# Kernel optimization log

Measured on AMD Instinct MI355X. Metric: run time of the kernel, lower is better.

The kernel has to match this reference:

```python
import jax, jax.numpy as jnp
import numpy as np

# dims: batch, samples, agents, obs_dim, action_dim, hidden
B, S, N, D, A, H = 512, 64, 8, 64, 16, 256
IN_DIM = (D + A) * N  # 640


def mish(x):
    return x * jnp.tanh(jax.nn.softplus(x))


def setup_inputs() -> dict:
    key = jax.random.key(0)
    ks = jax.random.split(key, 9)
    u = lambda k, shape, fan_in: jax.random.uniform(
        k, shape, jnp.float32, -1.0 / np.sqrt(fan_in), 1.0 / np.sqrt(fan_in))
    return {
        "state": jax.random.normal(ks[0], (B, N, D), jnp.float32),
        "action": jax.random.normal(ks[1], (B, N, A), jnp.float32),
        "W1": u(ks[2], (IN_DIM, H), IN_DIM),
        "b1": u(ks[3], (H,), IN_DIM),
        "W2": u(ks[4], (H, H), H),
        "b2": u(ks[5], (H,), H),
        "W3": u(ks[6], (H, 1), H),
        "b3": u(ks[7], (1,), H),
        # random grand-coalition permutations of the N agents, per (batch, sample)
        "perm": jnp.argsort(jax.random.uniform(ks[8], (B, S, N)), axis=-1).astype(jnp.int32),
    }


def reference(state, action, W1, b1, W2, b2, W3, b3, perm):
    # subcoalition mask [B,S,N,N]: torch builds one-hot(perm) @ tril(ones),
    # i.e. mask[b,s,i,j] = 1 iff j <= perm[b,s,i]
    subcoal = (jnp.arange(N) <= perm[..., None]).astype(state.dtype)
    # gathered actions in coalition order [B,S,N,A]: act_g[b,s,j] = action[b, perm[b,s,j]]
    act_g = action[jnp.arange(B)[:, None, None], perm]
    # masked subcoalition actions [B,S,N,N,A] -> [B,S,N,N*A]
    act = (act_g[:, :, None, :, :] * subcoal[..., None]).reshape(B, S, N, N * A)
    # flattened global obs broadcast over (sample, agent) axes [B,S,N,N*D]
    obs = jnp.broadcast_to(state.reshape(B, 1, 1, N * D), (B, S, N, N * D))
    x = jnp.concatenate([obs, act], axis=-1)  # [B,S,N,IN_DIM]
    # per-agent loop in torch uses shared q1 weights -> single batched MLP
    h = mish(x @ W1 + b1)
    h = mish(h @ W2 + b2)
    q = h @ W3 + b3                   # [B,S,N,1]
    q1 = q.mean(axis=1).squeeze(-1)   # mean over samples -> [B,N]
    return (q1, q1)
```

## Files before the change

### kernel.cpp

```cpp
#include <hip/hip_runtime.h>

typedef unsigned short ushort_t;
typedef _Float16 half_t;
typedef __attribute__((ext_vector_type(2))) _Float16 half2_t;
typedef __attribute__((ext_vector_type(8))) _Float16 half8_t;
typedef __attribute__((ext_vector_type(2))) __fp16 fp16x2;
typedef __attribute__((ext_vector_type(2))) float fx2;
typedef __attribute__((ext_vector_type(4))) float floatx4;

#define LOG2E 1.4426950408889634f
#define LN2   0.6931471805599453f

__device__ __forceinline__ float exp2_(float x) {
#if __has_builtin(__builtin_amdgcn_exp2f)
    return __builtin_amdgcn_exp2f(x);
#else
    return exp2f(x);
#endif
}

__device__ __forceinline__ half2_t cvt_pk_f16(float a, float b) {
    auto r = __builtin_amdgcn_cvt_pkrtz(a, b);
    return __builtin_bit_cast(half2_t, r);
}

__device__ __forceinline__ float fdot2_(half2_t a, half2_t b) {
#if __has_builtin(__builtin_amdgcn_fdot2)
    return __builtin_amdgcn_fdot2(__builtin_bit_cast(fp16x2, a),
                                  __builtin_bit_cast(fp16x2, b), 0.0f, false);
#else
    return (float)a.x * (float)b.x + (float)a.y * (float)b.y;
#endif
}

__device__ __forceinline__ fx2 mish2(fx2 t0) {
    fx2 one = {1.0f, 1.0f};
    fx2 m2  = {-2.0f, -2.0f};
    fx2 u   = {exp2_(t0.x), exp2_(t0.y)};
    fx2 s   = u + one;
    fx2 wv  = __builtin_elementwise_fma(s, s, one);
    fx2 rr  = {__builtin_amdgcn_rcpf(wv.x), __builtin_amdgcn_rcpf(wv.y)};
    fx2 v   = __builtin_elementwise_fma(rr, m2, one);
    return t0 * v;
}

__device__ __forceinline__ float dpp_sum16(float v) {
    int x = __float_as_int(v);
    v += __int_as_float(__builtin_amdgcn_update_dpp(0, x, 0xB1, 0xF, 0xF, true));
    x = __float_as_int(v);
    v += __int_as_float(__builtin_amdgcn_update_dpp(0, x, 0x4E, 0xF, 0xF, true));
    x = __float_as_int(v);
    v += __int_as_float(__builtin_amdgcn_update_dpp(0, x, 0x124, 0xF, 0xF, true));
    x = __float_as_int(v);
    v += __int_as_float(__builtin_amdgcn_update_dpp(0, x, 0x128, 0xF, 0xF, true));
    return v;
}

__global__ __launch_bounds__(256) void prep_kernel(
        const float* __restrict__ state,
        const float* __restrict__ action,
        const float* __restrict__ W1,
        const float* __restrict__ W2,
        float* __restrict__ obsWp,
        half_t* __restrict__ actW,
        half_t* __restrict__ W2T,
        float* __restrict__ out) {
    int bid = blockIdx.x;
    int t = threadIdx.x;
    if (bid < 512) {
        int bg = bid >> 3;
        int kc = bid & 7;
        int bs = bg * 8;
        const float* w1p = W1 + (size_t)(kc * 64) * 256 + t;
        const float* stp = state + (size_t)bs * 512 + kc * 64;
        float acc[8];
#pragma unroll
        for (int bb = 0; bb < 8; ++bb) acc[bb] = 0.f;
#pragma unroll 4
        for (int f = 0; f < 64; ++f) {
            float w = w1p[f * 256];
#pragma unroll
            for (int bb = 0; bb < 8; ++bb)
                acc[bb] = fmaf(stp[bb * 512 + f], w, acc[bb]);
        }
#pragma unroll
        for (int bb = 0; bb < 8; ++bb)
            obsWp[(size_t)kc * 131072 + (bs + bb) * 256 + t] = acc[bb];
    } else if (bid < 1536) {
        int idx = bid - 512;
        int j = idx & 7;
        int b0 = (idx >> 3) * 4;
        const float* W1a = W1 + (size_t)(512 + j * 16) * 256;
        float wv[16];
#pragma unroll
        for (int a = 0; a < 16; ++a) wv[a] = W1a[a * 256 + t];
#pragma unroll
        for (int bb = 0; bb < 4; ++bb) {
            int b = b0 + bb;
            const float* acp = action + (size_t)b * 128;
            float acc[8];
#pragma unroll
            for (int n = 0; n < 8; ++n) acc[n] = 0.f;
#pragma unroll
            for (int a = 0; a < 16; ++a) {
#pragma unroll
                for (int n = 0; n < 8; ++n)
                    acc[n] = fmaf(acp[n * 16 + a], wv[a], acc[n]);
            }
#pragma unroll
            for (int n = 0; n < 8; ++n)
                actW[(((size_t)b * 8 + n) * 8 + j) * 256 + t] = (half_t)(acc[n] * LOG2E);
        }
    } else {
        int blk = bid - 1536;
        if (blk < 16) {
            out[blk * 512 + t] = 0.0f;
            out[blk * 512 + 256 + t] = 0.0f;
        }
        int n = blk * 8 + (t >> 5);
        int klo = t & 31;
#pragma unroll
        for (int kk = 0; kk < 8; ++kk) {
            int k = kk * 32 + klo;
            W2T[n * 256 + k] = (half_t)W2[k * 256 + n];
        }
    }
}

#define CHUNK_US 528

__global__ __launch_bounds__(512, 4) void main_kernel(
        const float* __restrict__ obsWp, const half_t* __restrict__ actW,
        const half_t* __restrict__ W2T, const int* __restrict__ perm,
        const float* __restrict__ b1, const float* __restrict__ b2,
        const float* __restrict__ W3, const float* __restrict__ b3,
        float* __restrict__ out) {
    __shared__ __align__(16) ushort_t h1[2][32 * CHUNK_US];
    __shared__ __align__(16) float obsb[256];
    __shared__ int perm_s[128];
    __shared__ float qpart[2][8][64];

    int t = threadIdx.x;
    int bid = blockIdx.x;
    int b = (bid & 7) * 64 + ((bid >> 3) & 63);
    int sgp = bid >> 9;
    int s0 = sgp * 16;

    int w = t >> 6;
    int L = t & 63;
    int lo = L & 15;
    int q = L >> 4;

    if (t < 256) {
        float s = b1[t];
#pragma unroll
        for (int c = 0; c < 8; ++c) s += obsWp[(size_t)c * 131072 + b * 256 + t];
        obsb[t] = s * LOG2E;
    } else if (t < 384) {
        perm_s[t - 256] = perm[((size_t)b * 64 + s0) * 8 + (t - 256)];
    }

    const half_t* w2base = W2T + ((size_t)(w * 32 + lo)) * 256 + q * 8;
    half8_t bpre[4];
    bpre[0] = *reinterpret_cast<const half8_t*>(w2base + 0 * 4096 + 0 * 32);
    bpre[1] = *reinterpret_cast<const half8_t*>(w2base + 1 * 4096 + 0 * 32);
    bpre[2] = *reinterpret_cast<const half8_t*>(w2base + 0 * 4096 + 1 * 32);
    bpre[3] = *reinterpret_cast<const half8_t*>(w2base + 1 * 4096 + 1 * 32);

    int g = L >> 1;
    int ksg = g >> 2;
    int qq = g & 3;
    int halfsel = L & 1;
    const half_t* actb = actW + (size_t)b * 64 * 256;
    int dstoff = qq * 128 + halfsel * 4 + ksg * CHUNK_US
               + (w >> 1) * (8 * CHUNK_US) + (w & 1) * 64;

    __syncthreads();

    float4 ob = *reinterpret_cast<const float4*>(obsb + L * 4);

    {
        uint2 av[8];
#pragma unroll
        for (int j = 0; j < 8; ++j) {
            int p = perm_s[(0 * 8 + w) * 8 + j];
            unsigned po = __builtin_amdgcn_readfirstlane((unsigned)((p * 8 + j) * 256));
            av[j] = *reinterpret_cast<const uint2*>(actb + po + L * 4);
        }
        fx2 r01 = {ob.x, ob.y};
        fx2 r23 = {ob.z, ob.w};
        ushort_t* dst0 = h1[0] + dstoff;
#pragma unroll
        for (int j = 0; j < 8; ++j) {
            half2_t a0 = __builtin_bit_cast(half2_t, av[j].x);
            half2_t a1 = __builtin_bit_cast(half2_t, av[j].y);
            r01 += (fx2){(float)a0.x, (float)a0.y};
            r23 += (fx2){(float)a1.x, (float)a1.y};
            fx2 h01 = mish2(r01);
            fx2 h23 = mish2(r23);
            uint2 pk = make_uint2(__builtin_bit_cast(unsigned, cvt_pk_f16(h01.x, h01.y)),
                                  __builtin_bit_cast(unsigned, cvt_pk_f16(h23.x, h23.y)));
            *reinterpret_cast<uint2*>(dst0 + j * 8) = pk;
        }
    }
    __syncthreads();

    floatx4 acc0[4][2];
#pragma unroll
    for (int mt = 0; mt < 4; ++mt)
#pragma unroll
        for (int nt = 0; nt < 2; ++nt) acc0[mt][nt] = (floatx4){0.f, 0.f, 0.f, 0.f};
    {
        uint2 av[8];
#pragma unroll
        for (int j = 0; j < 8; ++j) {
            int p = perm_s[(1 * 8 + w) * 8 + j];
            unsigned po = __builtin_amdgcn_readfirstlane((unsigned)((p * 8 + j) * 256));
            av[j] = *reinterpret_cast<const uint2*>(actb + po + L * 4);
        }
        fx2 r01 = {ob.x, ob.y};
        fx2 r23 = {ob.z, ob.w};
        ushort_t* dst1 = h1[1] + dstoff;
        const ushort_t* h1b0 = h1[0] + L * 8;
#pragma unroll
        for (int ks = 0; ks < 8; ++ks) {
            half8_t afr[4];
#pragma unroll
            for (int mt = 0; mt < 4; ++mt)
                afr[mt] = *reinterpret_cast<const half8_t*>(h1b0 + (mt * 8 + ks) * CHUNK_US);
            half8_t bfr0 = (ks == 0) ? bpre[0] : (ks == 1) ? bpre[2]
                         : *reinterpret_cast<const half8_t*>(w2base + 0 * 4096 + ks * 32);
            half8_t bfr1 = (ks == 0) ? bpre[1] : (ks == 1) ? bpre[3]
                         : *reinterpret_cast<const half8_t*>(w2base + 1 * 4096 + ks * 32);
#pragma unroll
            for (int mt = 0; mt < 4; ++mt) {
                acc0[mt][0] = __builtin_amdgcn_mfma_f32_16x16x32_f16(afr[mt], bfr0, acc0[mt][0], 0, 0, 0);
                acc0[mt][1] = __builtin_amdgcn_mfma_f32_16x16x32_f16(afr[mt], bfr1, acc0[mt][1], 0, 0, 0);
            }
            {
                half2_t a0 = __builtin_bit_cast(half2_t, av[ks].x);
                half2_t a1 = __builtin_bit_cast(half2_t, av[ks].y);
                r01 += (fx2){(float)a0.x, (float)a0.y};
                r23 += (fx2){(float)a1.x, (float)a1.y};
                fx2 h01 = mish2(r01);
                fx2 h23 = mish2(r23);
                uint2 pk = make_uint2(__builtin_bit_cast(unsigned, cvt_pk_f16(h01.x, h01.y)),
                                      __builtin_bit_cast(unsigned, cvt_pk_f16(h23.x, h23.y)));
                *reinterpret_cast<uint2*>(dst1 + ks * 8) = pk;
            }
        }
    }
    __syncthreads();

    int col0 = w * 32 + 0 * 16 + lo;
    int col1 = w * 32 + 1 * 16 + lo;
    fx2 b2p = {b2[col0] * LOG2E, b2[col1] * LOG2E};
    half2_t w3p = cvt_pk_f16(W3[col0] * LN2, W3[col1] * LN2);

    floatx4 acc1[4][2];
#pragma unroll
    for (int mt = 0; mt < 4; ++mt)
#pragma unroll
        for (int nt = 0; nt < 2; ++nt) acc1[mt][nt] = (floatx4){0.f, 0.f, 0.f, 0.f};
    {
        const ushort_t* h1b1 = h1[1] + L * 8;
#pragma unroll
        for (int ks = 0; ks < 8; ++ks) {
            half8_t afr[4];
#pragma unroll
            for (int mt = 0; mt < 4; ++mt)
                afr[mt] = *reinterpret_cast<const half8_t*>(h1b1 + (mt * 8 + ks) * CHUNK_US);
            half8_t bfr0 = (ks == 0) ? bpre[0] : (ks == 1) ? bpre[2]
                         : *reinterpret_cast<const half8_t*>(w2base + 0 * 4096 + ks * 32);
            half8_t bfr1 = (ks == 0) ? bpre[1] : (ks == 1) ? bpre[3]
                         : *reinterpret_cast<const half8_t*>(w2base + 1 * 4096 + ks * 32);
#pragma unroll
            for (int mt = 0; mt < 4; ++mt) {
                acc1[mt][0] = __builtin_amdgcn_mfma_f32_16x16x32_f16(afr[mt], bfr0, acc1[mt][0], 0, 0, 0);
                acc1[mt][1] = __builtin_amdgcn_mfma_f32_16x16x32_f16(afr[mt], bfr1, acc1[mt][1], 0, 0, 0);
            }
#pragma unroll
            for (int v = 0; v < 2; ++v) {
                int idx = ks * 2 + v;
                int mt = idx >> 2, r = idx & 3;
                fx2 t2 = {acc0[mt][0][r], acc0[mt][1][r]};
                t2 += b2p;
                fx2 hh = mish2(t2);
                float part = fdot2_(cvt_pk_f16(hh.x, hh.y), w3p);
                float s = dpp_sum16(part);
                if (lo == 0) qpart[0][w][mt * 16 + q * 4 + r] = s;
            }
        }
    }
#pragma unroll
    for (int idx = 0; idx < 16; ++idx) {
        int mt = idx >> 2, r = idx & 3;
        fx2 t2 = {acc1[mt][0][r], acc1[mt][1][r]};
        t2 += b2p;
        fx2 hh = mish2(t2);
        float part = fdot2_(cvt_pk_f16(hh.x, hh.y), w3p);
        float s = dpp_sum16(part);
        if (lo == 0) qpart[1][w][mt * 16 + q * 4 + r] = s;
    }
    __syncthreads();

    if (t < 16) {
        int h = t >> 3, i = t & 7;
        float p = 0.f;
#pragma unroll
        for (int sl = 0; sl < 8; ++sl) {
            int k = perm_s[(h * 8 + sl) * 8 + i];
            int row = sl * 8 + k;
            float qv = b3[0];
#pragma unroll
            for (int ww = 0; ww < 8; ++ww) qv += qpart[h][ww][row];
            p += qv;
        }
        p *= (1.0f / 64.0f);
        atomicAdd(&out[b * 8 + i], p);
        atomicAdd(&out[4096 + b * 8 + i], p);
    }
}

extern "C" void kernel_launch(void* const* d_in, const int* in_sizes, int n_in,
                              void* d_out, int out_size, void* d_ws, size_t ws_size,
                              hipStream_t stream) {
    const float* state  = (const float*)d_in[0];
    const float* action = (const float*)d_in[1];
    const float* W1     = (const float*)d_in[2];
    const float* b1     = (const float*)d_in[3];
    const float* W2     = (const float*)d_in[4];
    const float* b2     = (const float*)d_in[5];
    const float* W3     = (const float*)d_in[6];
    const float* b3     = (const float*)d_in[7];
    const int*   perm   = (const int*)d_in[8];
    float* out = (float*)d_out;

    char* ws = (char*)d_ws;
    float*  obsWp = (float*)ws;
    half_t* actW  = (half_t*)(ws + 4194304);
    half_t* W2T   = (half_t*)(ws + 4194304 + 16777216);

    prep_kernel<<<1568, 256, 0, stream>>>(state, action, W1, W2, obsWp, actW, W2T, out);
    main_kernel<<<2048, 512, 0, stream>>>(obsWp, actW, W2T, perm, b1, b2, W3, b3, out);
}
```

Measured before the change: 164.4 us.

## Halve LDS tile and pipeline four sample groups to raise occupancy

Restructures the main kernel to process the 16 samples as four groups of 4 (32 rows) instead of two groups of 8, halving the h1 LDS double buffer. Layer-1 activation building, the layer-2 MFMA and the layer-3 epilogue of the previous group are overlapped in a software pipeline. Launch bounds rise to 6 blocks per CU, aiming for more waves resident to hide latency. The cost is more barriers, smaller MFMA tiles per wave with less reuse of W2 fragments (which are now reloaded each group and no longer prefetched), and narrower activation loads.

```diff
diff --git a/kernel.cpp b/kernel.cpp
--- a/kernel.cpp
+++ b/kernel.cpp
@@ -129,16 +129,16 @@
 
 #define CHUNK_US 528
 
-__global__ __launch_bounds__(512, 4) void main_kernel(
+__global__ __launch_bounds__(512, 6) void main_kernel(
         const float* __restrict__ obsWp, const half_t* __restrict__ actW,
         const half_t* __restrict__ W2T, const int* __restrict__ perm,
         const float* __restrict__ b1, const float* __restrict__ b2,
         const float* __restrict__ W3, const float* __restrict__ b3,
         float* __restrict__ out) {
-    __shared__ __align__(16) ushort_t h1[2][32 * CHUNK_US];
+    __shared__ __align__(16) ushort_t h1[2][16 * CHUNK_US];
     __shared__ __align__(16) float obsb[256];
     __shared__ int perm_s[128];
-    __shared__ float qpart[2][8][64];
+    __shared__ float qpart[4][8][32];
 
     int t = threadIdx.x;
     int bid = blockIdx.x;
@@ -149,7 +149,7 @@
     int w = t >> 6;
     int L = t & 63;
     int lo = L & 15;
-    int q = L >> 4;
+    int q4 = L >> 4;
 
     if (t < 256) {
         float s = b1[t];
@@ -160,165 +160,135 @@
         perm_s[t - 256] = perm[((size_t)b * 64 + s0) * 8 + (t - 256)];
     }
 
-    const half_t* w2base = W2T + ((size_t)(w * 32 + lo)) * 256 + q * 8;
-    half8_t bpre[4];
-    bpre[0] = *reinterpret_cast<const half8_t*>(w2base + 0 * 4096 + 0 * 32);
-    bpre[1] = *reinterpret_cast<const half8_t*>(w2base + 1 * 4096 + 0 * 32);
-    bpre[2] = *reinterpret_cast<const half8_t*>(w2base + 0 * 4096 + 1 * 32);
-    bpre[3] = *reinterpret_cast<const half8_t*>(w2base + 1 * 4096 + 1 * 32);
-
-    int g = L >> 1;
-    int ksg = g >> 2;
-    int qq = g & 3;
-    int halfsel = L & 1;
-    const half_t* actb = actW + (size_t)b * 64 * 256;
-    int dstoff = qq * 128 + halfsel * 4 + ksg * CHUNK_US
-               + (w >> 1) * (8 * CHUNK_US) + (w & 1) * 64;
-
-    __syncthreads();
-
-    float4 ob = *reinterpret_cast<const float4*>(obsb + L * 4);
-
-    {
-        uint2 av[8];
-#pragma unroll
-        for (int j = 0; j < 8; ++j) {
-            int p = perm_s[(0 * 8 + w) * 8 + j];
-            unsigned po = __builtin_amdgcn_readfirstlane((unsigned)((p * 8 + j) * 256));
-            av[j] = *reinterpret_cast<const uint2*>(actb + po + L * 4);
-        }
-        fx2 r01 = {ob.x, ob.y};
-        fx2 r23 = {ob.z, ob.w};
-        ushort_t* dst0 = h1[0] + dstoff;
-#pragma unroll
-        for (int j = 0; j < 8; ++j) {
-            half2_t a0 = __builtin_bit_cast(half2_t, av[j].x);
-            half2_t a1 = __builtin_bit_cast(half2_t, av[j].y);
-            r01 += (fx2){(float)a0.x, (float)a0.y};
-            r23 += (fx2){(float)a1.x, (float)a1.y};
-            fx2 h01 = mish2(r01);
-            fx2 h23 = mish2(r23);
-            uint2 pk = make_uint2(__builtin_bit_cast(unsigned, cvt_pk_f16(h01.x, h01.y)),
-                                  __builtin_bit_cast(unsigned, cvt_pk_f16(h23.x, h23.y)));
-            *reinterpret_cast<uint2*>(dst0 + j * 8) = pk;
-        }
-    }
-    __syncthreads();
-
-    floatx4 acc0[4][2];
-#pragma unroll
-    for (int mt = 0; mt < 4; ++mt)
-#pragma unroll
-        for (int nt = 0; nt < 2; ++nt) acc0[mt][nt] = (floatx4){0.f, 0.f, 0.f, 0.f};
-    {
-        uint2 av[8];
-#pragma unroll
-        for (int j = 0; j < 8; ++j) {
-            int p = perm_s[(1 * 8 + w) * 8 + j];
-            unsigned po = __builtin_amdgcn_readfirstlane((unsigned)((p * 8 + j) * 256));
-            av[j] = *reinterpret_cast<const uint2*>(actb + po + L * 4);
-        }
-        fx2 r01 = {ob.x, ob.y};
-        fx2 r23 = {ob.z, ob.w};
-        ushort_t* dst1 = h1[1] + dstoff;
-        const ushort_t* h1b0 = h1[0] + L * 8;
-#pragma unroll
-        for (int ks = 0; ks < 8; ++ks) {
-            half8_t afr[4];
-#pragma unroll
-            for (int mt = 0; mt < 4; ++mt)
-                afr[mt] = *reinterpret_cast<const half8_t*>(h1b0 + (mt * 8 + ks) * CHUNK_US);
-            half8_t bfr0 = (ks == 0) ? bpre[0] : (ks == 1) ? bpre[2]
-                         : *reinterpret_cast<const half8_t*>(w2base + 0 * 4096 + ks * 32);
-            half8_t bfr1 = (ks == 0) ? bpre[1] : (ks == 1) ? bpre[3]
-                         : *reinterpret_cast<const half8_t*>(w2base + 1 * 4096 + ks * 32);
-#pragma unroll
-            for (int mt = 0; mt < 4; ++mt) {
-                acc0[mt][0] = __builtin_amdgcn_mfma_f32_16x16x32_f16(afr[mt], bfr0, acc0[mt][0], 0, 0, 0);
-                acc0[mt][1] = __builtin_amdgcn_mfma_f32_16x16x32_f16(afr[mt], bfr1, acc0[mt][1], 0, 0, 0);
-            }
-            {
-                half2_t a0 = __builtin_bit_cast(half2_t, av[ks].x);
-                half2_t a1 = __builtin_bit_cast(half2_t, av[ks].y);
-                r01 += (fx2){(float)a0.x, (float)a0.y};
-                r23 += (fx2){(float)a1.x, (float)a1.y};
-                fx2 h01 = mish2(r01);
-                fx2 h23 = mish2(r23);
-                uint2 pk = make_uint2(__builtin_bit_cast(unsigned, cvt_pk_f16(h01.x, h01.y)),
-                                      __builtin_bit_cast(unsigned, cvt_pk_f16(h23.x, h23.y)));
-                *reinterpret_cast<uint2*>(dst1 + ks * 8) = pk;
-            }
-        }
-    }
-    __syncthreads();
+    const half_t* w2base = W2T + ((size_t)(w * 32 + lo)) * 256 + q4 * 8;
+
+    int s_loc = w & 3;
+    int ch = w >> 2;
+    int c0 = ch * 128 + L * 2;
+    int gks = ch * 4 + (L >> 4);
+    int gq = (L >> 2) & 3;
+    int lr_base = (s_loc & 1) * 8;
+    int mt_b = s_loc >> 1;
+    const half_t* actg = actW + (size_t)b * 64 * 256 + c0;
+    int dstoff = (mt_b * 8 + gks) * CHUNK_US + (gq * 16 + lr_base) * 8 + (L & 3) * 2;
 
     int col0 = w * 32 + 0 * 16 + lo;
     int col1 = w * 32 + 1 * 16 + lo;
     fx2 b2p = {b2[col0] * LOG2E, b2[col1] * LOG2E};
     half2_t w3p = cvt_pk_f16(W3[col0] * LN2, W3[col1] * LN2);
 
-    floatx4 acc1[4][2];
-#pragma unroll
-    for (int mt = 0; mt < 4; ++mt)
-#pragma unroll
-        for (int nt = 0; nt < 2; ++nt) acc1[mt][nt] = (floatx4){0.f, 0.f, 0.f, 0.f};
+    __syncthreads();
+
+    fx2 ob = {obsb[c0], obsb[c0 + 1]};
+
     {
-        const ushort_t* h1b1 = h1[1] + L * 8;
+        unsigned av[8];
+#pragma unroll
+        for (int j = 0; j < 8; ++j) {
+            int p = perm_s[s_loc * 8 + j];
+            av[j] = *reinterpret_cast<const unsigned*>(actg + (p * 8 + j) * 256);
+        }
+        fx2 r = ob;
+        ushort_t* dst = h1[0] + dstoff;
+#pragma unroll
+        for (int j = 0; j < 8; ++j) {
+            half2_t a0 = __builtin_bit_cast(half2_t, av[j]);
+            r += (fx2){(float)a0.x, (float)a0.y};
+            fx2 h = mish2(r);
+            *reinterpret_cast<unsigned*>(dst + j * 8) =
+                __builtin_bit_cast(unsigned, cvt_pk_f16(h.x, h.y));
+        }
+    }
+    __syncthreads();
+
+    floatx4 acc[2][2][2];
+
+#pragma unroll
+    for (int g = 0; g < 4; ++g) {
+        int cur = g & 1;
+        int nxt = cur ^ 1;
+#pragma unroll
+        for (int mt = 0; mt < 2; ++mt)
+#pragma unroll
+            for (int nt = 0; nt < 2; ++nt)
+                acc[cur][mt][nt] = (floatx4){0.f, 0.f, 0.f, 0.f};
+
+        unsigned av[8];
+        fx2 r;
+        if (g < 3) {
+#pragma unroll
+            for (int j = 0; j < 8; ++j) {
+                int p = perm_s[((g + 1) * 4 + s_loc) * 8 + j];
+                av[j] = *reinterpret_cast<const unsigned*>(actg + (p * 8 + j) * 256);
+            }
+            r = ob;
+        }
+        const ushort_t* h1b = h1[cur] + L * 8;
+        ushort_t* dst = h1[nxt] + dstoff;
+
 #pragma unroll
         for (int ks = 0; ks < 8; ++ks) {
-            half8_t afr[4];
-#pragma unroll
-            for (int mt = 0; mt < 4; ++mt)
-                afr[mt] = *reinterpret_cast<const half8_t*>(h1b1 + (mt * 8 + ks) * CHUNK_US);
-            half8_t bfr0 = (ks == 0) ? bpre[0] : (ks == 1) ? bpre[2]
-                         : *reinterpret_cast<const half8_t*>(w2base + 0 * 4096 + ks * 32);
-            half8_t bfr1 = (ks == 0) ? bpre[1] : (ks == 1) ? bpre[3]
-                         : *reinterpret_cast<const half8_t*>(w2base + 1 * 4096 + ks * 32);
-#pragma unroll
-            for (int mt = 0; mt < 4; ++mt) {
-                acc1[mt][0] = __builtin_amdgcn_mfma_f32_16x16x32_f16(afr[mt], bfr0, acc1[mt][0], 0, 0, 0);
-                acc1[mt][1] = __builtin_amdgcn_mfma_f32_16x16x32_f16(afr[mt], bfr1, acc1[mt][1], 0, 0, 0);
-            }
-#pragma unroll
-            for (int v = 0; v < 2; ++v) {
-                int idx = ks * 2 + v;
-                int mt = idx >> 2, r = idx & 3;
-                fx2 t2 = {acc0[mt][0][r], acc0[mt][1][r]};
+            half8_t afr[2];
+#pragma unroll
+            for (int mt = 0; mt < 2; ++mt)
+                afr[mt] = *reinterpret_cast<const half8_t*>(h1b + (mt * 8 + ks) * CHUNK_US);
+            half8_t bfr0 = *reinterpret_cast<const half8_t*>(w2base + 0 * 4096 + ks * 32);
+            half8_t bfr1 = *reinterpret_cast<const half8_t*>(w2base + 1 * 4096 + ks * 32);
+#pragma unroll
+            for (int mt = 0; mt < 2; ++mt) {
+                acc[cur][mt][0] = __builtin_amdgcn_mfma_f32_16x16x32_f16(afr[mt], bfr0, acc[cur][mt][0], 0, 0, 0);
+                acc[cur][mt][1] = __builtin_amdgcn_mfma_f32_16x16x32_f16(afr[mt], bfr1, acc[cur][mt][1], 0, 0, 0);
+            }
+            if (g < 3) {
+                half2_t a0 = __builtin_bit_cast(half2_t, av[ks]);
+                r += (fx2){(float)a0.x, (float)a0.y};
+                fx2 h = mish2(r);
+                *reinterpret_cast<unsigned*>(dst + ks * 8) =
+                    __builtin_bit_cast(unsigned, cvt_pk_f16(h.x, h.y));
+            }
+            if (g > 0) {
+                int prv = cur ^ 1;
+                int mt = ks >> 2, rr = ks & 3;
+                fx2 t2 = {acc[prv][mt][0][rr], acc[prv][mt][1][rr]};
                 t2 += b2p;
                 fx2 hh = mish2(t2);
                 float part = fdot2_(cvt_pk_f16(hh.x, hh.y), w3p);
-                float s = dpp_sum16(part);
-                if (lo == 0) qpart[0][w][mt * 16 + q * 4 + r] = s;
-            }
-        }
-    }
-#pragma unroll
-    for (int idx = 0; idx < 16; ++idx) {
-        int mt = idx >> 2, r = idx & 3;
-        fx2 t2 = {acc1[mt][0][r], acc1[mt][1][r]};
+                float sv = dpp_sum16(part);
+                if (lo == 0) qpart[g - 1][w][mt * 16 + q4 * 4 + rr] = sv;
+            }
+        }
+        __syncthreads();
+    }
+
+#pragma unroll
+    for (int ks = 0; ks < 8; ++ks) {
+        int mt = ks >> 2, rr = ks & 3;
+        fx2 t2 = {acc[1][mt][0][rr], acc[1][mt][1][rr]};
         t2 += b2p;
         fx2 hh = mish2(t2);
         float part = fdot2_(cvt_pk_f16(hh.x, hh.y), w3p);
-        float s = dpp_sum16(part);
-        if (lo == 0) qpart[1][w][mt * 16 + q * 4 + r] = s;
+        float sv = dpp_sum16(part);
+        if (lo == 0) qpart[3][w][mt * 16 + q4 * 4 + rr] = sv;
     }
     __syncthreads();
 
-    if (t < 16) {
-        int h = t >> 3, i = t & 7;
-        float p = 0.f;
-#pragma unroll
-        for (int sl = 0; sl < 8; ++sl) {
-            int k = perm_s[(h * 8 + sl) * 8 + i];
-            int row = sl * 8 + k;
-            float qv = b3[0];
-#pragma unroll
-            for (int ww = 0; ww < 8; ++ww) qv += qpart[h][ww][row];
-            p += qv;
-        }
-        p *= (1.0f / 64.0f);
-        atomicAdd(&out[b * 8 + i], p);
-        atomicAdd(&out[4096 + b * 8 + i], p);
+    if (t < 128) {
+        int si = t >> 3;
+        int i = t & 7;
+        int k = perm_s[si * 8 + i];
+        int row = (si & 3) * 8 + k;
+        int gg = si >> 2;
+        float qv = b3[0];
+#pragma unroll
+        for (int ww = 0; ww < 8; ++ww) qv += qpart[gg][ww][row];
+        qv += __shfl_xor(qv, 8);
+        qv += __shfl_xor(qv, 16);
+        qv += __shfl_xor(qv, 32);
+        if ((t & 63) < 8) {
+            float p = qv * (1.0f / 64.0f);
+            atomicAdd(&out[b * 8 + i], p);
+            atomicAdd(&out[4096 + b * 8 + i], p);
+        }
     }
 }
 
```

Result: slower. 226.4 us (+37.7%).
